# Optimization experiments

Measured on AMD Instinct MI355X. Metric: run time of the kernel, lower is better.

The kernel has to match this reference:

```python
import jax, jax.numpy as jnp
import numpy as np

MARGIN = 0.5
EPS = 1e-12  # matches torch F.normalize eps


def setup_inputs() -> dict:
    key = jax.random.key(0)
    embeddings = jax.random.normal(key, (8192, 256), dtype=jnp.float32)
    return {"embeddings": embeddings}


def reference(embeddings):
    n = embeddings.shape[0]
    # L2-normalize rows (torch F.normalize: x / max(||x||, eps))
    norm = jnp.linalg.norm(embeddings, axis=1, keepdims=True)
    e = embeddings / jnp.maximum(norm, EPS)
    sim = e @ e.T  # [n, n]
    # strict upper triangle mask (i < j)
    iu = jnp.triu(jnp.ones((n, n), dtype=bool), k=1)
    loss_sum = jnp.sum(jnp.where(iu, jax.nn.relu(sim - MARGIN), 0.0))
    count = n * (n - 1) // 2
    return loss_sum / count
```

## Files before the change

kernel.cpp:

```cpp
#include <hip/hip_runtime.h>
#include <hip/hip_fp16.h>

typedef __attribute__((ext_vector_type(4))) float f32x4;
typedef __attribute__((ext_vector_type(8))) int i32x8;

#define NROWS 8192
#define DCOLS 256
#define MARGIN 0.5f
#define NT 64
#define NBLOCKS 544

__global__ __launch_bounds__(256) void norm_kernel(const float* __restrict__ x,
                                                   unsigned char* __restrict__ e) {
    const int t = threadIdx.x;
    const int l = t & 63;
    const int c = l & 31;
    const int row = blockIdx.x * 8 + (t >> 6) * 2 + (l >> 5);

    const float4 v0 = *reinterpret_cast<const float4*>(&x[row * DCOLS + c * 8]);
    const float4 v1 = *reinterpret_cast<const float4*>(&x[row * DCOLS + c * 8 + 4]);
    float ss = v0.x * v0.x + v0.y * v0.y + v0.z * v0.z + v0.w * v0.w
             + v1.x * v1.x + v1.y * v1.y + v1.z * v1.z + v1.w * v1.w;
#pragma unroll
    for (int off = 16; off >= 1; off >>= 1) ss += __shfl_xor(ss, off, 32);
    const float inv = 1.0f / fmaxf(sqrtf(ss), 1e-12f);

    const float f[8] = {v0.x, v0.y, v0.z, v0.w, v1.x, v1.y, v1.z, v1.w};
    unsigned int lo = 0, hi = 0;
#pragma unroll
    for (int i = 0; i < 4; ++i) {
        const unsigned short hb = __half_as_ushort(__float2half(f[i] * inv));
        lo |= (unsigned int)(hb >> 8) << (8 * i);
    }
#pragma unroll
    for (int i = 0; i < 4; ++i) {
        const unsigned short hb = __half_as_ushort(__float2half(f[4 + i] * inv));
        hi |= (unsigned int)(hb >> 8) << (8 * i);
    }
    uint2 o; o.x = lo; o.y = hi;
    *reinterpret_cast<uint2*>(e + (size_t)row * DCOLS + c * 8) = o;
}

__global__ __launch_bounds__(256, 2) void tile_kernel(const unsigned char* __restrict__ e,
                                                      float* __restrict__ part) {
    const int orig = blockIdx.x;
    int bb = (orig & 7) * 68 + (orig >> 3);
    int bi = 0;
    while (bb >= ((NT - bi) + 3) >> 2) { bb -= ((NT - bi) + 3) >> 2; ++bi; }
    const int j0 = bi + bb * 4;
    const int nj = min(4, NT - j0);
    const int NS = nj * 2;

    __shared__ char lds[65536];
    char* As = lds;
    char* Bw = lds + 16384;
    float* red = (float*)lds;

    const int t = threadIdx.x;
    const int l = t & 63;
    const int w = t >> 6;
    const int wn = w;
    const int lr = l & 15;
    const int hk = l >> 4;
    const unsigned char* eA = e + (size_t)bi * 128 * DCOLS;
    const unsigned char* eB = e + (size_t)j0 * 128 * DCOLS + wn * 32 * DCOLS;
    char* myB = Bw + w * 12288;

    auto stageB = [&](int stream, int slot) {
#pragma unroll
        for (int i = 0; i < 4; ++i) {
            const int u = i * 64 + l;
            const int shk = (u >> 6) & 3, srow = (u >> 1) & 31, sc = u & 1;
            __builtin_amdgcn_global_load_lds(
                (const __attribute__((address_space(1))) void*)(eB
                    + (size_t)(stream >> 1) * 128 * DCOLS
                    + srow * DCOLS + (stream & 1) * 128 + shk * 32 + sc * 16),
                (__attribute__((address_space(3))) void*)(myB + slot * 4096 + u * 16),
                16, 0, 0);
        }
    };

#pragma unroll
    for (int i = 0; i < 4; ++i) {
        const int u = i * 256 + t;
        const int shk = (u >> 8) & 3, srow = (u >> 1) & 127, sc = u & 1;
        __builtin_amdgcn_global_load_lds(
            (const __attribute__((address_space(1))) void*)(eA + srow * DCOLS + shk * 32 + sc * 16),
            (__attribute__((address_space(3))) void*)(As + u * 16), 16, 0, 0);
    }
    stageB(0, 0);
    stageB(1, 1);
    asm volatile("s_waitcnt vmcnt(8)" ::: "memory");
    __builtin_amdgcn_s_barrier();
    __builtin_amdgcn_sched_barrier(0);

    i32x8 af[2][8];
#pragma unroll
    for (int m = 0; m < 8; ++m)
        af[0][m] = *reinterpret_cast<const i32x8*>(As + hk * 4096 + (m * 16 + lr) * 32);
    __builtin_amdgcn_s_barrier();
    __builtin_amdgcn_sched_barrier(0);
#pragma unroll
    for (int i = 0; i < 4; ++i) {
        const int u = i * 256 + t;
        const int shk = (u >> 8) & 3, srow = (u >> 1) & 127, sc = u & 1;
        __builtin_amdgcn_global_load_lds(
            (const __attribute__((address_space(1))) void*)(eA + srow * DCOLS + 128 + shk * 32 + sc * 16),
            (__attribute__((address_space(3))) void*)(As + u * 16), 16, 0, 0);
    }
    asm volatile("s_waitcnt vmcnt(0)" ::: "memory");
    __builtin_amdgcn_s_barrier();
    __builtin_amdgcn_sched_barrier(0);
#pragma unroll
    for (int m = 0; m < 8; ++m)
        af[1][m] = *reinterpret_cast<const i32x8*>(As + hk * 4096 + (m * 16 + lr) * 32);

    f32x4 acc[8][2];
#pragma unroll
    for (int m = 0; m < 8; ++m)
#pragma unroll
        for (int n = 0; n < 2; ++n)
            acc[m][n] = (f32x4){0.f, 0.f, 0.f, 0.f};

    float local = 0.0f;
    for (int jx = 0; jx < nj; ++jx) {
        const int jt = j0 + jx;
#pragma unroll
        for (int kb = 0; kb < 2; ++kb) {
            const int s = jx * 2 + kb;
            asm volatile("s_waitcnt vmcnt(4)" ::: "memory");
            {
                int s2 = s + 2; if (s2 >= NS) s2 -= NS;
                int slot = s + 2; while (slot >= 3) slot -= 3;
                stageB(s2, slot);
            }
            int slotc = s; while (slotc >= 3) slotc -= 3;
            i32x8 bf[2];
#pragma unroll
            for (int n = 0; n < 2; ++n)
                bf[n] = *reinterpret_cast<const i32x8*>(
                    myB + slotc * 4096 + hk * 1024 + (n * 16 + lr) * 32);
            __builtin_amdgcn_s_setprio(1);
#pragma unroll
            for (int m = 0; m < 8; ++m)
#pragma unroll
                for (int n = 0; n < 2; ++n)
                    acc[m][n] = __builtin_amdgcn_mfma_scale_f32_16x16x128_f8f6f4(
                        af[kb][m], bf[n], acc[m][n],
                        1, 1,
                        0, 0x7F7F7F7F,
                        0, 0x7F7F7F7F);
            __builtin_amdgcn_s_setprio(0);
        }
        const int gi0 = bi * 128;
        const int gj0 = jt * 128 + wn * 32;
        if (jt == bi) {
#pragma unroll
            for (int m = 0; m < 8; ++m)
#pragma unroll
                for (int n = 0; n < 2; ++n) {
#pragma unroll
                    for (int r = 0; r < 4; ++r) {
                        const int gi = gi0 + m * 16 + hk * 4 + r;
                        const int gj = gj0 + n * 16 + lr;
                        local += (gi < gj) ? fmaxf(acc[m][n][r] - MARGIN, 0.0f) : 0.0f;
                    }
                    acc[m][n] = (f32x4){0.f, 0.f, 0.f, 0.f};
                }
        } else {
#pragma unroll
            for (int m = 0; m < 8; ++m)
#pragma unroll
                for (int n = 0; n < 2; ++n) {
#pragma unroll
                    for (int r = 0; r < 4; ++r)
                        local += fmaxf(acc[m][n][r] - MARGIN, 0.0f);
                    acc[m][n] = (f32x4){0.f, 0.f, 0.f, 0.f};
                }
        }
    }

#pragma unroll
    for (int off = 32; off >= 1; off >>= 1) local += __shfl_down(local, off);
    __syncthreads();
    if (l == 0) red[w] = local;
    __syncthreads();
    if (t == 0) part[orig] = red[0] + red[1] + red[2] + red[3];
}

__global__ __launch_bounds__(256) void fin_kernel(const float* __restrict__ part,
                                                  float* __restrict__ out) {
    __shared__ float red[4];
    const int t = threadIdx.x;
    float v = part[t] + part[t + 256] + (t < NBLOCKS - 512 ? part[t + 512] : 0.0f);
#pragma unroll
    for (int off = 32; off >= 1; off >>= 1) v += __shfl_down(v, off);
    if ((t & 63) == 0) red[t >> 6] = v;
    __syncthreads();
    if (t == 0) out[0] = (red[0] + red[1] + red[2] + red[3]) / 33550336.0f;
}

extern "C" void kernel_launch(void* const* d_in, const int* in_sizes, int n_in,
                              void* d_out, int out_size, void* d_ws, size_t ws_size,
                              hipStream_t stream) {
    const float* x = (const float*)d_in[0];
    float* out = (float*)d_out;
    unsigned char* e = (unsigned char*)d_ws;
    float* part = (float*)((char*)d_ws + (size_t)NROWS * DCOLS);

    norm_kernel<<<NROWS / 8, 256, 0, stream>>>(x, e);
    tile_kernel<<<NBLOCKS, 256, 0, stream>>>(e, part);
    fin_kernel<<<1, 256, 0, stream>>>(part, out);
}
```

Baseline: 30.75 us.

## Split A row-tiles into 64-row bands, double-buffer B, raise occupancy

```diff
diff --git a/kernel.cpp b/kernel.cpp
--- a/kernel.cpp
+++ b/kernel.cpp
@@ -7,8 +7,9 @@
 #define NROWS 8192
 #define DCOLS 256
 #define MARGIN 0.5f
-#define NT 64
-#define NBLOCKS 544
+#define NBAND 128
+#define NCT 64
+#define NBLOCKS 1088
 
 __global__ __launch_bounds__(256) void norm_kernel(const float* __restrict__ x,
                                                    unsigned char* __restrict__ e) {
@@ -41,20 +42,19 @@
     *reinterpret_cast<uint2*>(e + (size_t)row * DCOLS + c * 8) = o;
 }
 
-__global__ __launch_bounds__(256, 2) void tile_kernel(const unsigned char* __restrict__ e,
+__global__ __launch_bounds__(256, 4) void tile_kernel(const unsigned char* __restrict__ e,
                                                       float* __restrict__ part) {
     const int orig = blockIdx.x;
-    int bb = (orig & 7) * 68 + (orig >> 3);
-    int bi = 0;
-    while (bb >= ((NT - bi) + 3) >> 2) { bb -= ((NT - bi) + 3) >> 2; ++bi; }
-    const int j0 = bi + bb * 4;
-    const int nj = min(4, NT - j0);
+    int bb = (orig & 7) * 136 + (orig >> 3);
+    int bi = 0, r;
+    while (bb >= (r = ((NCT - (bi >> 1)) + 3) >> 2)) { bb -= r; ++bi; }
+    const int j0 = (bi >> 1) + bb * 4;
+    const int nj = min(4, NCT - j0);
     const int NS = nj * 2;
 
-    __shared__ char lds[65536];
+    __shared__ char lds[40960];
     char* As = lds;
-    char* Bw = lds + 16384;
-    float* red = (float*)lds;
+    char* Bw = lds + 8192;
 
     const int t = threadIdx.x;
     const int l = t & 63;
@@ -62,62 +62,57 @@
     const int wn = w;
     const int lr = l & 15;
     const int hk = l >> 4;
-    const unsigned char* eA = e + (size_t)bi * 128 * DCOLS;
-    const unsigned char* eB = e + (size_t)j0 * 128 * DCOLS + wn * 32 * DCOLS;
-    char* myB = Bw + w * 12288;
-
-    auto stageB = [&](int stream, int slot) {
+    const unsigned char* eA = e + (size_t)bi * 64 * DCOLS;
+    char* myB = Bw + w * 8192;
+
+    auto stageB = [&](int s, int slot) {
+        const int jt = j0 + (s >> 1);
+        const int kb = s & 1;
+        const unsigned char* src = e + (size_t)(jt * 128 + wn * 32) * DCOLS + kb * 128;
 #pragma unroll
         for (int i = 0; i < 4; ++i) {
             const int u = i * 64 + l;
-            const int shk = (u >> 6) & 3, srow = (u >> 1) & 31, sc = u & 1;
+            const int hk2 = u >> 6, brow = (u >> 1) & 31, half = u & 1;
             __builtin_amdgcn_global_load_lds(
-                (const __attribute__((address_space(1))) void*)(eB
-                    + (size_t)(stream >> 1) * 128 * DCOLS
-                    + srow * DCOLS + (stream & 1) * 128 + shk * 32 + sc * 16),
-                (__attribute__((address_space(3))) void*)(myB + slot * 4096 + u * 16),
-                16, 0, 0);
+                (const __attribute__((address_space(1))) void*)(src + brow * DCOLS + hk2 * 32 + half * 16),
+                (__attribute__((address_space(3))) void*)(myB + slot * 4096 + u * 16), 16, 0, 0);
         }
     };
-
-#pragma unroll
-    for (int i = 0; i < 4; ++i) {
-        const int u = i * 256 + t;
-        const int shk = (u >> 8) & 3, srow = (u >> 1) & 127, sc = u & 1;
-        __builtin_amdgcn_global_load_lds(
-            (const __attribute__((address_space(1))) void*)(eA + srow * DCOLS + shk * 32 + sc * 16),
-            (__attribute__((address_space(3))) void*)(As + u * 16), 16, 0, 0);
-    }
+    auto stageA = [&](int kb) {
+#pragma unroll
+        for (int i = 0; i < 2; ++i) {
+            const int u = i * 256 + t;
+            const int hk2 = u >> 7, arow = (u >> 1) & 63, half = u & 1;
+            __builtin_amdgcn_global_load_lds(
+                (const __attribute__((address_space(1))) void*)(eA + arow * DCOLS + kb * 128 + hk2 * 32 + half * 16),
+                (__attribute__((address_space(3))) void*)(As + u * 16), 16, 0, 0);
+        }
+    };
+
+    stageA(0);
     stageB(0, 0);
     stageB(1, 1);
     asm volatile("s_waitcnt vmcnt(8)" ::: "memory");
     __builtin_amdgcn_s_barrier();
     __builtin_amdgcn_sched_barrier(0);
 
-    i32x8 af[2][8];
-#pragma unroll
-    for (int m = 0; m < 8; ++m)
-        af[0][m] = *reinterpret_cast<const i32x8*>(As + hk * 4096 + (m * 16 + lr) * 32);
+    i32x8 af[2][4];
+#pragma unroll
+    for (int m = 0; m < 4; ++m)
+        af[0][m] = *reinterpret_cast<const i32x8*>(As + hk * 2048 + (m * 16 + lr) * 32);
     __builtin_amdgcn_s_barrier();
     __builtin_amdgcn_sched_barrier(0);
-#pragma unroll
-    for (int i = 0; i < 4; ++i) {
-        const int u = i * 256 + t;
-        const int shk = (u >> 8) & 3, srow = (u >> 1) & 127, sc = u & 1;
-        __builtin_amdgcn_global_load_lds(
-            (const __attribute__((address_space(1))) void*)(eA + srow * DCOLS + 128 + shk * 32 + sc * 16),
-            (__attribute__((address_space(3))) void*)(As + u * 16), 16, 0, 0);
-    }
+    stageA(1);
     asm volatile("s_waitcnt vmcnt(0)" ::: "memory");
     __builtin_amdgcn_s_barrier();
     __builtin_amdgcn_sched_barrier(0);
 #pragma unroll
-    for (int m = 0; m < 8; ++m)
-        af[1][m] = *reinterpret_cast<const i32x8*>(As + hk * 4096 + (m * 16 + lr) * 32);
-
-    f32x4 acc[8][2];
-#pragma unroll
-    for (int m = 0; m < 8; ++m)
+    for (int m = 0; m < 4; ++m)
+        af[1][m] = *reinterpret_cast<const i32x8*>(As + hk * 2048 + (m * 16 + lr) * 32);
+
+    f32x4 acc[4][2];
+#pragma unroll
+    for (int m = 0; m < 4; ++m)
 #pragma unroll
         for (int n = 0; n < 2; ++n)
             acc[m][n] = (f32x4){0.f, 0.f, 0.f, 0.f};
@@ -129,20 +124,17 @@
         for (int kb = 0; kb < 2; ++kb) {
             const int s = jx * 2 + kb;
             asm volatile("s_waitcnt vmcnt(4)" ::: "memory");
-            {
-                int s2 = s + 2; if (s2 >= NS) s2 -= NS;
-                int slot = s + 2; while (slot >= 3) slot -= 3;
-                stageB(s2, slot);
-            }
-            int slotc = s; while (slotc >= 3) slotc -= 3;
             i32x8 bf[2];
 #pragma unroll
             for (int n = 0; n < 2; ++n)
                 bf[n] = *reinterpret_cast<const i32x8*>(
-                    myB + slotc * 4096 + hk * 1024 + (n * 16 + lr) * 32);
+                    myB + (s & 1) * 4096 + hk * 1024 + (n * 16 + lr) * 32);
+            asm volatile("s_waitcnt lgkmcnt(0)" ::: "memory");
+            __builtin_amdgcn_sched_barrier(0);
+            if (s + 2 < NS) stageB(s + 2, s & 1);
             __builtin_amdgcn_s_setprio(1);
 #pragma unroll
-            for (int m = 0; m < 8; ++m)
+            for (int m = 0; m < 4; ++m)
 #pragma unroll
                 for (int n = 0; n < 2; ++n)
                     acc[m][n] = __builtin_amdgcn_mfma_scale_f32_16x16x128_f8f6f4(
@@ -152,29 +144,29 @@
                         0, 0x7F7F7F7F);
             __builtin_amdgcn_s_setprio(0);
         }
-        const int gi0 = bi * 128;
+        const int gi0 = bi * 64;
         const int gj0 = jt * 128 + wn * 32;
-        if (jt == bi) {
-#pragma unroll
-            for (int m = 0; m < 8; ++m)
+        if (jt == (bi >> 1)) {
+#pragma unroll
+            for (int m = 0; m < 4; ++m)
 #pragma unroll
                 for (int n = 0; n < 2; ++n) {
 #pragma unroll
-                    for (int r = 0; r < 4; ++r) {
-                        const int gi = gi0 + m * 16 + hk * 4 + r;
+                    for (int r2 = 0; r2 < 4; ++r2) {
+                        const int gi = gi0 + m * 16 + hk * 4 + r2;
                         const int gj = gj0 + n * 16 + lr;
-                        local += (gi < gj) ? fmaxf(acc[m][n][r] - MARGIN, 0.0f) : 0.0f;
+                        local += (gi < gj) ? fmaxf(acc[m][n][r2] - MARGIN, 0.0f) : 0.0f;
                     }
                     acc[m][n] = (f32x4){0.f, 0.f, 0.f, 0.f};
                 }
         } else {
 #pragma unroll
-            for (int m = 0; m < 8; ++m)
+            for (int m = 0; m < 4; ++m)
 #pragma unroll
                 for (int n = 0; n < 2; ++n) {
 #pragma unroll
-                    for (int r = 0; r < 4; ++r)
-                        local += fmaxf(acc[m][n][r] - MARGIN, 0.0f);
+                    for (int r2 = 0; r2 < 4; ++r2)
+                        local += fmaxf(acc[m][n][r2] - MARGIN, 0.0f);
                     acc[m][n] = (f32x4){0.f, 0.f, 0.f, 0.f};
                 }
         }
@@ -183,6 +175,7 @@
 #pragma unroll
     for (int off = 32; off >= 1; off >>= 1) local += __shfl_down(local, off);
     __syncthreads();
+    float* red = (float*)lds;
     if (l == 0) red[w] = local;
     __syncthreads();
     if (t == 0) part[orig] = red[0] + red[1] + red[2] + red[3];
@@ -192,7 +185,8 @@
                                                   float* __restrict__ out) {
     __shared__ float red[4];
     const int t = threadIdx.x;
-    float v = part[t] + part[t + 256] + (t < NBLOCKS - 512 ? part[t + 512] : 0.0f);
+    float v = part[t] + part[t + 256] + part[t + 512] + part[t + 768]
+            + (t < NBLOCKS - 1024 ? part[t + 1024] : 0.0f);
 #pragma unroll
     for (int off = 32; off >= 1; off >>= 1) v += __shfl_down(v, off);
     if ((t & 63) == 0) red[t >> 6] = v;
```

Result: slower. 33.00 us (+7.3%).
